# Kernel optimization log

Measured on AMD Instinct MI355X. Metric: run time of the kernel, lower is better.

Reference implementation:

```python
import jax, jax.numpy as jnp
import numpy as np
from jax import lax

L = 64          # filter_length
C = 64          # n_channels
B = 64          # batch
T = 4096        # time steps per call


def _sliding_max(a, k):
    # a: [B, C, T + k - 1] -> [B, C, T], windowed max, stride 1, VALID
    return lax.reduce_window(a, -jnp.inf, lax.max, (1, 1, k), (1, 1, 1), 'VALID')


def setup_inputs() -> dict:
    key = jax.random.key(0)
    x = jax.random.normal(key, (B, C, T), dtype=jnp.float32)
    # State buffers as lazily allocated by the module on first forward:
    prev_input = jnp.full((B, C, L - 1), -jnp.inf, dtype=jnp.float32)
    prev_max_out = jnp.full((B, C, L - 1), jnp.inf, dtype=jnp.float32)
    return {'x': x, 'prev_input': prev_input, 'prev_max_out': prev_max_out}


def reference(x, prev_input, prev_max_out):
    # max-pool over [prev_input, x] with kernel L, stride 1 (causal streaming max)
    max_input = jnp.concatenate([prev_input, x], axis=-1)        # [B, C, T+L-1]
    max_out = _sliding_max(max_input, L)                         # [B, C, T]
    # min-pool over [prev_max_out, max_out] via negated max-pool
    min_input = jnp.concatenate([prev_max_out, max_out], axis=-1)  # [B, C, T+L-1]
    out = -_sliding_max(-min_input, L)                           # [B, C, T]
    return out
```

## Files before the change

kernel.cpp:

```cpp
#include <hip/hip_runtime.h>
#include <math.h>


#define TT   4096
#define PADN 63
#define SLEN 4160

template<int CTRL>
__device__ __forceinline__ float dpp_self(float v) {
  return __int_as_float(__builtin_amdgcn_update_dpp(
      __float_as_int(v), __float_as_int(v), CTRL, 0xF, 0xF, false));
}
template<int CTRL>
__device__ __forceinline__ float dpp_old(float oldv, float v) {
  return __int_as_float(__builtin_amdgcn_update_dpp(
      __float_as_int(oldv), __float_as_int(v), CTRL, 0xF, 0xF, false));
}

template<bool IS_MAX>
__device__ __forceinline__ void chunk_windows(const float* sbuf, int b, int lane,
                                              float r[4], float& u_out) {
  const float ID = IS_MAX ? -INFINITY : INFINITY;
#define OPF(x, y) (IS_MAX ? fmaxf((x), (y)) : fminf((x), (y)))
  const float4 a0 = *reinterpret_cast<const float4*>(sbuf + b + 4 * lane);
  const float4 a1 = *reinterpret_cast<const float4*>(sbuf + b + 64 + 4 * lane);

  float s3 = a0.w;
  float s2 = OPF(a0.z, s3);
  float s1 = OPF(a0.y, s2);
  float s0 = OPF(a0.x, s1);
  float t = s0;
  t = OPF(t, dpp_self<0x101>(t));
  t = OPF(t, dpp_self<0x102>(t));
  t = OPF(t, dpp_self<0x104>(t));
  t = OPF(t, dpp_self<0x108>(t));
  float E = dpp_old<0x101>(ID, t);

  float p0 = a1.x;
  float p1 = OPF(p0, a1.y);
  float p2 = OPF(p1, a1.z);
  float p3 = OPF(p2, a1.w);
  float u = p3;
  u = OPF(u, dpp_self<0x111>(u));
  u = OPF(u, dpp_self<0x112>(u));
  u = OPF(u, dpp_self<0x114>(u));
  u = OPF(u, dpp_self<0x118>(u));
  float Ep = dpp_old<0x111>(ID, u);

  r[0] = OPF(OPF(s0, E), Ep);
  r[1] = OPF(OPF(s1, E), OPF(Ep, p0));
  r[2] = OPF(OPF(s2, E), OPF(Ep, p1));
  r[3] = OPF(OPF(s3, E), OPF(Ep, p2));
  u_out = u;
#undef OPF
}

__global__ __launch_bounds__(512)
void mmh_kernel(const float* __restrict__ x,
                const float* __restrict__ prev_input,
                const float* __restrict__ prev_max_out,
                float* __restrict__ out)
{
    __shared__ float s_in[SLEN];
    __shared__ float s_mid[SLEN];

    const int row  = blockIdx.x;
    const int tid  = threadIdx.x;
    const int lane = tid & 63;
    const int wave = tid >> 6;

    const float* xrow  = x            + (size_t)row * TT;
    const float* pirow = prev_input   + (size_t)row * PADN;
    const float* pmrow = prev_max_out + (size_t)row * PADN;
    float*       orow  = out          + (size_t)row * TT;

    for (int i = tid; i < 1023; i += 512) {
        float4 v = *reinterpret_cast<const float4*>(xrow + 4 * i);
        float  e = xrow[4 * i + 4];
        float4 w = make_float4(v.y, v.z, v.w, e);
        *reinterpret_cast<float4*>(&s_in[64 + 4 * i]) = w;
    }
    if (tid < 63)       { s_in[tid] = pirow[tid]; s_mid[tid] = pmrow[tid]; }
    else if (tid == 63) { s_in[63] = xrow[0]; }
    else if (tid < 67)  { s_in[4156 + tid - 64] = xrow[4093 + tid - 64]; }
    else if (tid == 67) { s_in[4159] = -INFINITY; }
    else if (tid == 68) { s_mid[4159] = INFINITY; }
    __syncthreads();

    #pragma unroll
    for (int cc = 0; cc < 2; ++cc) {
        const int b = (wave + 8 * cc) << 8;
        float r[4], u;
        chunk_windows<true>(s_in, b, lane, r, u);
        float  w3 = dpp_old<0x101>(u, r[0]);
        float4 wv = make_float4(r[1], r[2], r[3], w3);
        *reinterpret_cast<float4*>(&s_mid[64 + b + 4 * lane]) = wv;
        if ((b | lane) == 0) s_mid[63] = r[0];
    }
    __syncthreads();

    #pragma unroll
    for (int cc = 0; cc < 2; ++cc) {
        const int b = (wave + 8 * cc) << 8;
        float r[4], u;
        chunk_windows<false>(s_mid, b, lane, r, u);
        *reinterpret_cast<float4*>(orow + b + 4 * lane) =
            make_float4(r[0], r[1], r[2], r[3]);
    }
}

extern "C" void kernel_launch(void* const* d_in, const int* in_sizes, int n_in,
                              void* d_out, int out_size, void* d_ws, size_t ws_size,
                              hipStream_t stream) {
    const float* x            = (const float*)d_in[0];
    const float* prev_input   = (const float*)d_in[1];
    const float* prev_max_out = (const float*)d_in[2];
    float*       out          = (float*)d_out;

    mmh_kernel<<<64 * 64, 512, 0, stream>>>(x, prev_input, prev_max_out, out);
}
```

Baseline: 116.5 us.

## Drop LDS staging; compute both pooling stages from direct global loads in registers

Result: slower. 126.9 us (+9.0%).

```diff
diff --git a/kernel.cpp b/kernel.cpp
--- a/kernel.cpp
+++ b/kernel.cpp
@@ -2,9 +2,11 @@
 #include <math.h>
 
 
-#define TT   4096
-#define PADN 63
-#define SLEN 4160
+#define TT    4096
+#define PADN  63
+#define XPMAX 4158
+
+struct __attribute__((packed, aligned(4))) f4u { float x, y, z, w; };
 
 template<int CTRL>
 __device__ __forceinline__ float dpp_self(float v) {
@@ -18,13 +20,9 @@
 }
 
 template<bool IS_MAX>
-__device__ __forceinline__ void chunk_windows(const float* sbuf, int b, int lane,
-                                              float r[4], float& u_out) {
+__device__ __forceinline__ void chunk_windows(float4 a0, float4 a1, float r[4]) {
   const float ID = IS_MAX ? -INFINITY : INFINITY;
 #define OPF(x, y) (IS_MAX ? fmaxf((x), (y)) : fminf((x), (y)))
-  const float4 a0 = *reinterpret_cast<const float4*>(sbuf + b + 4 * lane);
-  const float4 a1 = *reinterpret_cast<const float4*>(sbuf + b + 64 + 4 * lane);
-
   float s3 = a0.w;
   float s2 = OPF(a0.z, s3);
   float s1 = OPF(a0.y, s2);
@@ -51,62 +49,74 @@
   r[1] = OPF(OPF(s1, E), OPF(Ep, p0));
   r[2] = OPF(OPF(s2, E), OPF(Ep, p1));
   r[3] = OPF(OPF(s3, E), OPF(Ep, p2));
-  u_out = u;
 #undef OPF
 }
 
-__global__ __launch_bounds__(512)
+__device__ __forceinline__ float4 load_slab(int t0, int l16,
+                                            const float* __restrict__ xrow,
+                                            const float* __restrict__ pirow) {
+  if (t0 >= PADN && t0 <= TT - 1) {
+    f4u v = *reinterpret_cast<const f4u*>(xrow + t0 - PADN + 4 * l16);
+    return make_float4(v.x, v.y, v.z, v.w);
+  }
+  float e[4];
+  #pragma unroll
+  for (int k = 0; k < 4; ++k) {
+    const int q = t0 + 4 * l16 + k;
+    float v;
+    if (q < 0)           v = -INFINITY;
+    else if (q < PADN)   v = pirow[q];
+    else if (q <= XPMAX) v = xrow[q - PADN];
+    else                 v = -INFINITY;
+    e[k] = v;
+  }
+  return make_float4(e[0], e[1], e[2], e[3]);
+}
+
+__global__ __launch_bounds__(256)
 void mmh_kernel(const float* __restrict__ x,
                 const float* __restrict__ prev_input,
                 const float* __restrict__ prev_max_out,
                 float* __restrict__ out)
 {
-    __shared__ float s_in[SLEN];
-    __shared__ float s_mid[SLEN];
-
-    const int row  = blockIdx.x;
     const int tid  = threadIdx.x;
     const int lane = tid & 63;
-    const int wave = tid >> 6;
+    const int wv   = tid >> 6;
+    const int l16  = lane & 15;
+    const int rrow = lane >> 4;
+
+    const int row   = blockIdx.x >> 2;
+    const int wbase = ((blockIdx.x & 3) * 4 + wv) * 256;
+    const int qA    = wbase + 64 * rrow;
 
     const float* xrow  = x            + (size_t)row * TT;
     const float* pirow = prev_input   + (size_t)row * PADN;
     const float* pmrow = prev_max_out + (size_t)row * PADN;
     float*       orow  = out          + (size_t)row * TT;
 
-    for (int i = tid; i < 1023; i += 512) {
-        float4 v = *reinterpret_cast<const float4*>(xrow + 4 * i);
-        float  e = xrow[4 * i + 4];
-        float4 w = make_float4(v.y, v.z, v.w, e);
-        *reinterpret_cast<float4*>(&s_in[64 + 4 * i]) = w;
+    const float4 X0 = load_slab(qA - 63, l16, xrow, pirow);
+    const float4 X1 = load_slab(qA + 1,  l16, xrow, pirow);
+    const float4 X2 = load_slab(qA + 65, l16, xrow, pirow);
+
+    float mA[4], mB[4];
+    chunk_windows<true>(X0, X1, mA);
+    chunk_windows<true>(X1, X2, mB);
+
+    if (qA == 0) {
+        #pragma unroll
+        for (int k = 0; k < 4; ++k) {
+            const int p = 4 * l16 + k;
+            if (p < PADN) mA[k] = pmrow[p];
+        }
     }
-    if (tid < 63)       { s_in[tid] = pirow[tid]; s_mid[tid] = pmrow[tid]; }
-    else if (tid == 63) { s_in[63] = xrow[0]; }
-    else if (tid < 67)  { s_in[4156 + tid - 64] = xrow[4093 + tid - 64]; }
-    else if (tid == 67) { s_in[4159] = -INFINITY; }
-    else if (tid == 68) { s_mid[4159] = INFINITY; }
-    __syncthreads();
 
-    #pragma unroll
-    for (int cc = 0; cc < 2; ++cc) {
-        const int b = (wave + 8 * cc) << 8;
-        float r[4], u;
-        chunk_windows<true>(s_in, b, lane, r, u);
-        float  w3 = dpp_old<0x101>(u, r[0]);
-        float4 wv = make_float4(r[1], r[2], r[3], w3);
-        *reinterpret_cast<float4*>(&s_mid[64 + b + 4 * lane]) = wv;
-        if ((b | lane) == 0) s_mid[63] = r[0];
-    }
-    __syncthreads();
+    const float4 a0 = make_float4(mA[0], mA[1], mA[2], mA[3]);
+    const float4 a1 = make_float4(mB[0], mB[1], mB[2], mB[3]);
+    float r[4];
+    chunk_windows<false>(a0, a1, r);
 
-    #pragma unroll
-    for (int cc = 0; cc < 2; ++cc) {
-        const int b = (wave + 8 * cc) << 8;
-        float r[4], u;
-        chunk_windows<false>(s_mid, b, lane, r, u);
-        *reinterpret_cast<float4*>(orow + b + 4 * lane) =
-            make_float4(r[0], r[1], r[2], r[3]);
-    }
+    *reinterpret_cast<float4*>(orow + qA + 4 * l16) =
+        make_float4(r[0], r[1], r[2], r[3]);
 }
 
 extern "C" void kernel_launch(void* const* d_in, const int* in_sizes, int n_in,
@@ -117,5 +127,5 @@
     const float* prev_max_out = (const float*)d_in[2];
     float*       out          = (float*)d_out;
 
-    mmh_kernel<<<64 * 64, 512, 0, stream>>>(x, prev_input, prev_max_out, out);
+    mmh_kernel<<<64 * 64 * 4, 256, 0, stream>>>(x, prev_input, prev_max_out, out);
 }
```
